# Kernel tuning notes

Hardware: AMD Instinct MI355X
Metric: run time of the kernel (lower is better)

Reference implementation:

```python
import jax, jax.numpy as jnp
import numpy as np

HEAD_DIM = 128
NEG = -1e9


def setup_inputs() -> dict:
    key = jax.random.key(0)
    kq, kk, kv, kl = jax.random.split(key, 4)
    B, S, D = 8, 2048, HEAD_DIM
    q = jax.random.normal(kq, (B, S, D), dtype=jnp.float32)
    k = jax.random.normal(kk, (B, S, D), dtype=jnp.float32)
    v = jax.random.normal(kv, (B, S, D), dtype=jnp.float32)
    event_length = jax.random.randint(kl, (B,), 0, 2048, dtype=jnp.int32)
    return {"q": q, "k": k, "v": v, "event_length": event_length}


def reference(q, k, v, event_length):
    B, S, D = q.shape
    scale = jnp.sqrt(jnp.asarray(D, dtype=q.dtype))
    # [B, S, S] attention scores
    scores = jnp.einsum("bsd,btd->bst", q, k) / scale
    idx = jnp.arange(S)
    valid = idx[None, :] < event_length[:, None]          # [B, S]
    mask = valid[:, :, None] & valid[:, None, :]          # [B, S, S]
    scores = jnp.where(mask, scores, jnp.asarray(NEG, dtype=scores.dtype))
    attn = jax.nn.softmax(scores, axis=-1)
    # dropout is eval-mode identity
    return jnp.einsum("bst,btd->bsd", attn, v)
```

## Files before the change

kernel.cpp:

```cpp
#include <hip/hip_runtime.h>

#define S 2048
#define D 128
#define BATCH 8
#define KSTR 136
#define VSTR 72

typedef _Float16 half8 __attribute__((ext_vector_type(8)));
typedef _Float16 half4_t __attribute__((ext_vector_type(4)));
typedef float f4 __attribute__((ext_vector_type(4)));

__device__ __forceinline__ half8 cvt8(f4 a, f4 b) {
    half8 h;
    h[0] = (_Float16)a[0]; h[1] = (_Float16)a[1];
    h[2] = (_Float16)a[2]; h[3] = (_Float16)a[3];
    h[4] = (_Float16)b[0]; h[5] = (_Float16)b[1];
    h[6] = (_Float16)b[2]; h[7] = (_Float16)b[3];
    return h;
}

__global__ __launch_bounds__(256) void k_prep(const float* __restrict__ kin,
                                              const float* __restrict__ v,
                                              _Float16* __restrict__ kh,
                                              _Float16* __restrict__ vt,
                                              float* __restrict__ sums) {
    int bid = blockIdx.x;
    int b = bid & 7, c = bid >> 3, tid = threadIdx.x;
    size_t off = ((size_t)b * S + c * 64) * D;
    #pragma unroll
    for (int p = 0; p < 4; ++p) {
        size_t i = (size_t)p * 2048 + tid * 8;
        f4 a = *(const f4*)(kin + off + i);
        f4 bb = *(const f4*)(kin + off + i + 4);
        *(half8*)(kh + off + i) = cvt8(a, bb);
    }
    __shared__ float tile[64 * 132];
    __shared__ f4 sred[256][2];
    f4 a0 = {0.f, 0.f, 0.f, 0.f}, a1 = {0.f, 0.f, 0.f, 0.f};
    int d0 = (tid & 15) * 8;
    #pragma unroll
    for (int p = 0; p < 4; ++p) {
        int t = p * 16 + (tid >> 4);
        f4 x = *(const f4*)(v + off + (size_t)t * D + d0);
        f4 y = *(const f4*)(v + off + (size_t)t * D + d0 + 4);
        a0 += x; a1 += y;
        *(f4*)&tile[t * 132 + d0] = x;
        *(f4*)&tile[t * 132 + d0 + 4] = y;
    }
    sred[tid][0] = a0; sred[tid][1] = a1;
    __syncthreads();
    if (tid < 16) {
        f4 s0 = sred[tid][0], s1 = sred[tid][1];
        for (int g = 1; g < 16; ++g) { s0 += sred[g * 16 + tid][0]; s1 += sred[g * 16 + tid][1]; }
        float* dst = sums + b * D + tid * 8;
        #pragma unroll
        for (int i = 0; i < 4; ++i) { atomicAdd(dst + i, s0[i]); atomicAdd(dst + 4 + i, s1[i]); }
    }
    int u = tid & 7, dd = tid >> 3;
    #pragma unroll
    for (int pass = 0; pass < 4; ++pass) {
        int d = pass * 32 + dd;
        half8 h;
        #pragma unroll
        for (int i = 0; i < 8; ++i) h[i] = (_Float16)tile[(u * 8 + i) * 132 + d];
        *(half8*)(vt + ((size_t)(b * D + d)) * S + c * 64 + u * 8) = h;
    }
}

__global__ __launch_bounds__(256, 2) void k_attn(
    const float* __restrict__ q, const _Float16* __restrict__ kh,
    const _Float16* __restrict__ vt, const int* __restrict__ el,
    const float* __restrict__ sums, float* __restrict__ out) {
    int bid = blockIdx.x;
    int b = bid & 7, mg = bid >> 3;
    int Lb = el[b], m0 = mg * 64;
    int tid = threadIdx.x;
    const float inv_s = 1.0f / (float)S;

    if (m0 >= Lb) {
        int r = tid >> 2, d0 = (tid & 3) * 32;
        float* orow = out + ((size_t)b * S + m0 + r) * D + d0;
        #pragma unroll
        for (int sg = 0; sg < 8; ++sg)
            *(f4*)(orow + sg * 4) = *(const f4*)(sums + b * D + d0 + sg * 4) * inv_s;
        return;
    }
    int nkt = (Lb + 63) >> 6;

    int lane = tid & 63, w = tid >> 6;
    int col = lane & 15, quad = lane >> 4;

    __shared__ _Float16 Kh[64 * KSTR];
    __shared__ _Float16 Vt[128 * VSTR];

    const float scale = 0.0883883476483184f;
    half8 qf[4];
    {
        const float* qb = q + ((size_t)b * S + m0 + w * 16 + col) * D;
        #pragma unroll
        for (int kc = 0; kc < 4; ++kc) {
            f4 a = *(const f4*)(qb + kc * 32 + quad * 8);
            f4 b2 = *(const f4*)(qb + kc * 32 + quad * 8 + 4);
            a *= scale; b2 *= scale;
            qf[kc] = cvt8(a, b2);
        }
    }

    f4 O[8];
    #pragma unroll
    for (int i = 0; i < 8; ++i) O[i] = (f4){0.f, 0.f, 0.f, 0.f};
    float ps = 0.f;

    int kr = tid >> 4, kc8 = (tid & 15) << 3;
    int vr = tid >> 3, vc8 = (tid & 7) << 3;
    const _Float16* kb_ = kh + (size_t)b * S * D;
    const _Float16* vb_ = vt + (size_t)b * D * S;

    half8 kreg[4], vreg[4];
    {
        #pragma unroll
        for (int p = 0; p < 4; ++p)
            kreg[p] = *(const half8*)(kb_ + (size_t)(p * 16 + kr) * D + kc8);
        #pragma unroll
        for (int p = 0; p < 4; ++p)
            vreg[p] = *(const half8*)(vb_ + (size_t)(p * 32 + vr) * S + vc8);
        #pragma unroll
        for (int p = 0; p < 4; ++p)
            *(half8*)&Kh[(p * 16 + kr) * KSTR + kc8] = kreg[p];
        #pragma unroll
        for (int p = 0; p < 4; ++p)
            *(half8*)&Vt[(p * 32 + vr) * VSTR + vc8] = vreg[p];
    }
    __syncthreads();

    for (int kt = 0; kt < nkt; ++kt) {
        int t0 = kt * 64;
        bool hasnext = (kt + 1) < nkt;
        if (hasnext) {
            int tn = t0 + 64;
            #pragma unroll
            for (int p = 0; p < 4; ++p)
                kreg[p] = *(const half8*)(kb_ + (size_t)(tn + p * 16 + kr) * D + kc8);
            #pragma unroll
            for (int p = 0; p < 4; ++p)
                vreg[p] = *(const half8*)(vb_ + (size_t)(p * 32 + vr) * S + tn + vc8);
        }

        #pragma unroll
        for (int nt = 0; nt < 4; ++nt) {
            f4 sa = {0.f, 0.f, 0.f, 0.f};
            __builtin_amdgcn_s_setprio(1);
            #pragma unroll
            for (int kc = 0; kc < 4; ++kc) {
                half8 kf = *(const half8*)&Kh[(nt * 16 + col) * KSTR + kc * 32 + quad * 8];
                sa = __builtin_amdgcn_mfma_f32_16x16x32_f16(kf, qf[kc], sa, 0, 0, 0);
            }
            __builtin_amdgcn_s_setprio(0);
            int tq = t0 + nt * 16 + quad * 4;
            half4_t ph;
            #pragma unroll
            for (int r = 0; r < 4; ++r) {
                float e = (tq + r < Lb) ? __expf(fminf(sa[r], 10.0f)) : 0.f;
                ps += e;
                ph[r] = (_Float16)e;
            }
            __builtin_amdgcn_s_setprio(1);
            #pragma unroll
            for (int dt = 0; dt < 8; ++dt) {
                half4_t vf = *(const half4_t*)&Vt[(dt * 16 + col) * VSTR + nt * 16 + quad * 4];
                O[dt] = __builtin_amdgcn_mfma_f32_16x16x16f16(ph, vf, O[dt], 0, 0, 0);
            }
            __builtin_amdgcn_s_setprio(0);
        }

        if (hasnext) {
            __syncthreads();
            #pragma unroll
            for (int p = 0; p < 4; ++p)
                *(half8*)&Kh[(p * 16 + kr) * KSTR + kc8] = kreg[p];
            #pragma unroll
            for (int p = 0; p < 4; ++p)
                *(half8*)&Vt[(p * 32 + vr) * VSTR + vc8] = vreg[p];
            __syncthreads();
        }
    }

    ps += __shfl_xor(ps, 16, 64);
    ps += __shfl_xor(ps, 32, 64);
    float l4[4];
    #pragma unroll
    for (int r = 0; r < 4; ++r) l4[r] = __shfl(ps, quad * 4 + r, 64);

    bool tail = (m0 + 64 > Lb);
    float smv[8] = {};
    if (tail) {
        #pragma unroll
        for (int dt = 0; dt < 8; ++dt) smv[dt] = sums[b * D + dt * 16 + col] * inv_s;
    }
    #pragma unroll
    for (int r = 0; r < 4; ++r) {
        int row = m0 + w * 16 + quad * 4 + r;
        float inv = 1.0f / l4[r];
        float* orow = out + ((size_t)b * S + row) * D;
        #pragma unroll
        for (int dt = 0; dt < 8; ++dt) {
            float val = (row < Lb) ? O[dt][r] * inv : smv[dt];
            orow[dt * 16 + col] = val;
        }
    }
}

extern "C" void kernel_launch(void* const* d_in, const int* in_sizes, int n_in,
                              void* d_out, int out_size, void* d_ws, size_t ws_size,
                              hipStream_t stream) {
    const float* q = (const float*)d_in[0];
    const float* k = (const float*)d_in[1];
    const float* v = (const float*)d_in[2];
    const int* el = (const int*)d_in[3];
    float* out = (float*)d_out;

    const size_t SZ_SUMS = 4096;
    const size_t SZ_HALF = (size_t)BATCH * D * S * 2;
    float* sums = (float*)d_ws;
    _Float16* kh = (_Float16*)((char*)d_ws + SZ_SUMS);
    _Float16* vt = (_Float16*)((char*)d_ws + SZ_SUMS + SZ_HALF);

    hipMemsetAsync(d_ws, 0, SZ_SUMS, stream);
    k_prep<<<dim3(256), 256, 0, stream>>>(k, v, kh, vt, sums);
    k_attn<<<dim3(256), 256, 0, stream>>>(q, kh, vt, el, sums, out);
}
```

Baseline: 128.6 us.

## Split attention key tile across two wave groups and combine partial outputs

The attention kernel now launches 512 threads per block. Two groups of four waves each process half of every 64-key tile, and their partial O accumulators and row sums are merged through shared memory at the end. This raises the number of waves per query block to hide MFMA and exp latency, at the cost of an extra shared-memory reduction and larger LDS use. The prep kernel is also split into twice as many smaller blocks.

```diff
diff --git a/kernel.cpp b/kernel.cpp
--- a/kernel.cpp
+++ b/kernel.cpp
@@ -26,20 +26,20 @@
                                               float* __restrict__ sums) {
     int bid = blockIdx.x;
     int b = bid & 7, c = bid >> 3, tid = threadIdx.x;
-    size_t off = ((size_t)b * S + c * 64) * D;
-    #pragma unroll
-    for (int p = 0; p < 4; ++p) {
+    size_t off = ((size_t)b * S + c * 32) * D;
+    #pragma unroll
+    for (int p = 0; p < 2; ++p) {
         size_t i = (size_t)p * 2048 + tid * 8;
         f4 a = *(const f4*)(kin + off + i);
         f4 bb = *(const f4*)(kin + off + i + 4);
         *(half8*)(kh + off + i) = cvt8(a, bb);
     }
-    __shared__ float tile[64 * 132];
+    __shared__ float tile[32 * 132];
     __shared__ f4 sred[256][2];
     f4 a0 = {0.f, 0.f, 0.f, 0.f}, a1 = {0.f, 0.f, 0.f, 0.f};
     int d0 = (tid & 15) * 8;
     #pragma unroll
-    for (int p = 0; p < 4; ++p) {
+    for (int p = 0; p < 2; ++p) {
         int t = p * 16 + (tid >> 4);
         f4 x = *(const f4*)(v + off + (size_t)t * D + d0);
         f4 y = *(const f4*)(v + off + (size_t)t * D + d0 + 4);
@@ -56,18 +56,18 @@
         #pragma unroll
         for (int i = 0; i < 4; ++i) { atomicAdd(dst + i, s0[i]); atomicAdd(dst + 4 + i, s1[i]); }
     }
-    int u = tid & 7, dd = tid >> 3;
-    #pragma unroll
-    for (int pass = 0; pass < 4; ++pass) {
-        int d = pass * 32 + dd;
+    int u = tid & 3, dd = tid >> 2;
+    #pragma unroll
+    for (int pass = 0; pass < 2; ++pass) {
+        int d = pass * 64 + dd;
         half8 h;
         #pragma unroll
         for (int i = 0; i < 8; ++i) h[i] = (_Float16)tile[(u * 8 + i) * 132 + d];
-        *(half8*)(vt + ((size_t)(b * D + d)) * S + c * 64 + u * 8) = h;
-    }
-}
-
-__global__ __launch_bounds__(256, 2) void k_attn(
+        *(half8*)(vt + ((size_t)(b * D + d)) * S + c * 32 + u * 8) = h;
+    }
+}
+
+__global__ __launch_bounds__(512, 2) void k_attn(
     const float* __restrict__ q, const _Float16* __restrict__ kh,
     const _Float16* __restrict__ vt, const int* __restrict__ el,
     const float* __restrict__ sums, float* __restrict__ out) {
@@ -78,25 +78,29 @@
     const float inv_s = 1.0f / (float)S;
 
     if (m0 >= Lb) {
-        int r = tid >> 2, d0 = (tid & 3) * 32;
+        int r = tid >> 3, d0 = (tid & 7) * 16;
         float* orow = out + ((size_t)b * S + m0 + r) * D + d0;
         #pragma unroll
-        for (int sg = 0; sg < 8; ++sg)
+        for (int sg = 0; sg < 4; ++sg)
             *(f4*)(orow + sg * 4) = *(const f4*)(sums + b * D + d0 + sg * 4) * inv_s;
         return;
     }
     int nkt = (Lb + 63) >> 6;
 
     int lane = tid & 63, w = tid >> 6;
+    int h = w >> 2, wl = w & 3;
     int col = lane & 15, quad = lane >> 4;
 
-    __shared__ _Float16 Kh[64 * KSTR];
-    __shared__ _Float16 Vt[128 * VSTR];
+    __shared__ __align__(16) char smem[35840];
+    _Float16* Kh = (_Float16*)smem;
+    _Float16* Vt = (_Float16*)(smem + 17408);
+    float* cmb = (float*)smem;
+    float* psb = (float*)(smem + 33792);
 
     const float scale = 0.0883883476483184f;
     half8 qf[4];
     {
-        const float* qb = q + ((size_t)b * S + m0 + w * 16 + col) * D;
+        const float* qb = q + ((size_t)b * S + m0 + wl * 16 + col) * D;
         #pragma unroll
         for (int kc = 0; kc < 4; ++kc) {
             f4 a = *(const f4*)(qb + kc * 32 + quad * 8);
@@ -116,20 +120,20 @@
     const _Float16* kb_ = kh + (size_t)b * S * D;
     const _Float16* vb_ = vt + (size_t)b * D * S;
 
-    half8 kreg[4], vreg[4];
+    half8 kreg[2], vreg[2];
     {
         #pragma unroll
-        for (int p = 0; p < 4; ++p)
-            kreg[p] = *(const half8*)(kb_ + (size_t)(p * 16 + kr) * D + kc8);
-        #pragma unroll
-        for (int p = 0; p < 4; ++p)
-            vreg[p] = *(const half8*)(vb_ + (size_t)(p * 32 + vr) * S + vc8);
-        #pragma unroll
-        for (int p = 0; p < 4; ++p)
-            *(half8*)&Kh[(p * 16 + kr) * KSTR + kc8] = kreg[p];
-        #pragma unroll
-        for (int p = 0; p < 4; ++p)
-            *(half8*)&Vt[(p * 32 + vr) * VSTR + vc8] = vreg[p];
+        for (int p = 0; p < 2; ++p)
+            kreg[p] = *(const half8*)(kb_ + (size_t)(p * 32 + kr) * D + kc8);
+        #pragma unroll
+        for (int p = 0; p < 2; ++p)
+            vreg[p] = *(const half8*)(vb_ + (size_t)(p * 64 + vr) * S + vc8);
+        #pragma unroll
+        for (int p = 0; p < 2; ++p)
+            *(half8*)&Kh[(p * 32 + kr) * KSTR + kc8] = kreg[p];
+        #pragma unroll
+        for (int p = 0; p < 2; ++p)
+            *(half8*)&Vt[(p * 64 + vr) * VSTR + vc8] = vreg[p];
     }
     __syncthreads();
 
@@ -139,15 +143,16 @@
         if (hasnext) {
             int tn = t0 + 64;
             #pragma unroll
-            for (int p = 0; p < 4; ++p)
-                kreg[p] = *(const half8*)(kb_ + (size_t)(tn + p * 16 + kr) * D + kc8);
-            #pragma unroll
-            for (int p = 0; p < 4; ++p)
-                vreg[p] = *(const half8*)(vb_ + (size_t)(p * 32 + vr) * S + tn + vc8);
-        }
-
-        #pragma unroll
-        for (int nt = 0; nt < 4; ++nt) {
+            for (int p = 0; p < 2; ++p)
+                kreg[p] = *(const half8*)(kb_ + (size_t)(tn + p * 32 + kr) * D + kc8);
+            #pragma unroll
+            for (int p = 0; p < 2; ++p)
+                vreg[p] = *(const half8*)(vb_ + (size_t)(p * 64 + vr) * S + tn + vc8);
+        }
+
+        #pragma unroll
+        for (int nt2 = 0; nt2 < 2; ++nt2) {
+            int nt = h * 2 + nt2;
             f4 sa = {0.f, 0.f, 0.f, 0.f};
             __builtin_amdgcn_s_setprio(1);
             #pragma unroll
@@ -176,36 +181,52 @@
         if (hasnext) {
             __syncthreads();
             #pragma unroll
-            for (int p = 0; p < 4; ++p)
-                *(half8*)&Kh[(p * 16 + kr) * KSTR + kc8] = kreg[p];
-            #pragma unroll
-            for (int p = 0; p < 4; ++p)
-                *(half8*)&Vt[(p * 32 + vr) * VSTR + vc8] = vreg[p];
+            for (int p = 0; p < 2; ++p)
+                *(half8*)&Kh[(p * 32 + kr) * KSTR + kc8] = kreg[p];
+            #pragma unroll
+            for (int p = 0; p < 2; ++p)
+                *(half8*)&Vt[(p * 64 + vr) * VSTR + vc8] = vreg[p];
             __syncthreads();
         }
     }
 
+    __syncthreads();
     ps += __shfl_xor(ps, 16, 64);
     ps += __shfl_xor(ps, 32, 64);
-    float l4[4];
-    #pragma unroll
-    for (int r = 0; r < 4; ++r) l4[r] = __shfl(ps, quad * 4 + r, 64);
-
-    bool tail = (m0 + 64 > Lb);
-    float smv[8] = {};
-    if (tail) {
-        #pragma unroll
-        for (int dt = 0; dt < 8; ++dt) smv[dt] = sums[b * D + dt * 16 + col] * inv_s;
-    }
-    #pragma unroll
-    for (int r = 0; r < 4; ++r) {
-        int row = m0 + w * 16 + quad * 4 + r;
-        float inv = 1.0f / l4[r];
-        float* orow = out + ((size_t)b * S + row) * D;
-        #pragma unroll
-        for (int dt = 0; dt < 8; ++dt) {
-            float val = (row < Lb) ? O[dt][r] * inv : smv[dt];
-            orow[dt * 16 + col] = val;
+
+    if (h == 1) {
+        #pragma unroll
+        for (int dt = 0; dt < 8; ++dt)
+            #pragma unroll
+            for (int r = 0; r < 4; ++r)
+                cmb[(wl * 16 + quad * 4 + r) * 132 + dt * 16 + col] = O[dt][r];
+        if (quad == 0) psb[wl * 16 + col] = ps;
+    }
+    __syncthreads();
+    if (h == 0) {
+        float pst = ps + psb[wl * 16 + col];
+        float l4[4];
+        #pragma unroll
+        for (int r = 0; r < 4; ++r) l4[r] = __shfl(pst, quad * 4 + r, 64);
+
+        bool tail = (m0 + 64 > Lb);
+        float smv[8] = {};
+        if (tail) {
+            #pragma unroll
+            for (int dt = 0; dt < 8; ++dt) smv[dt] = sums[b * D + dt * 16 + col] * inv_s;
+        }
+        #pragma unroll
+        for (int r = 0; r < 4; ++r) {
+            int row = m0 + wl * 16 + quad * 4 + r;
+            float inv = 1.0f / l4[r];
+            float* orow = out + ((size_t)b * S + row) * D;
+            #pragma unroll
+            for (int dt = 0; dt < 8; ++dt) {
+                float val = (row < Lb)
+                    ? (O[dt][r] + cmb[(wl * 16 + quad * 4 + r) * 132 + dt * 16 + col]) * inv
+                    : smv[dt];
+                orow[dt * 16 + col] = val;
+            }
         }
     }
 }
@@ -226,6 +247,6 @@
     _Float16* vt = (_Float16*)((char*)d_ws + SZ_SUMS + SZ_HALF);
 
     hipMemsetAsync(d_ws, 0, SZ_SUMS, stream);
-    k_prep<<<dim3(256), 256, 0, stream>>>(k, v, kh, vt, sums);
-    k_attn<<<dim3(256), 256, 0, stream>>>(q, kh, vt, el, sums, out);
-}
+    k_prep<<<dim3(512), 256, 0, stream>>>(k, v, kh, vt, sums);
+    k_attn<<<dim3(256), 512, 0, stream>>>(q, kh, vt, el, sums, out);
+}
```

After: 123.6 us. 3.9% less time.
